# Kernel tuning notes

Measured on AMD Instinct MI355X. Metric: run time of the kernel, lower is better.

The kernel has to match this reference:

```python
import jax, jax.numpy as jnp
import numpy as np

I = 512   # input_size
H = 512   # hidden_size
NH = 2    # num_layers - 1 hidden cells
B = 8
S = 4096

def _unif(k, shape, fan_in):
    bound = 1.0 / np.sqrt(fan_in)
    return jax.random.uniform(k, shape, jnp.float32, -bound, bound)

def setup_inputs() -> dict:
    key = jax.random.key(0)
    ks = jax.random.split(key, 13)
    return {
        "xs": jax.random.normal(ks[0], (B, S, I), jnp.float32),
        # input cell
        "W_xh0": _unif(ks[1], (H, I), I), "b_xh0": _unif(ks[2], (H,), I),
        "W_hh0": _unif(ks[3], (H, H), H), "b_hh0": _unif(ks[4], (H,), H),
        "W_hy0": _unif(ks[5], (H, H), H), "b_hy0": _unif(ks[6], (H,), H),
        # hidden cells, stacked [NH, ...]
        "W_xh_h": _unif(ks[7], (NH, H, H), H), "b_xh_h": _unif(ks[8], (NH, H), H),
        "W_hh_h": _unif(ks[9], (NH, H, H), H), "b_hh_h": _unif(ks[10], (NH, H), H),
        "W_hy_h": _unif(ks[11], (NH, H, H), H), "b_hy_h": _unif(ks[12], (NH, H), H),
    }

def reference(xs, W_xh0, b_xh0, W_hh0, b_hh0, W_hy0, b_hy0,
              W_xh_h, b_xh_h, W_hh_h, b_hh_h, W_hy_h, b_hy_h):
    # NOTE: the original torch forward never passes hs back into the input
    # cell across timesteps (hs is re-zeroed each step), so timesteps are
    # fully independent and we process all (B*S) tokens at once.
    b, s, i = xs.shape
    x = xs.reshape(b * s, i)
    # input cell: hs=0 so W_hh contributes only its bias
    h = jnp.tanh(x @ W_xh0.T + b_xh0 + b_hh0)
    y = h @ W_hy0.T + b_hy0
    # hidden cells (dropout p=0.0 -> identity)
    for li in range(W_xh_h.shape[0]):
        h = jnp.tanh(h @ W_hh_h[li].T + b_hh_h[li] + y @ W_xh_h[li].T + b_xh_h[li])
        y = h @ W_hy_h[li].T + b_hy_h[li]
    outputs = y.reshape(b, s, -1).transpose(1, 0, 2)      # [S, B, H] like torch.stack
    hs_final = h.reshape(b, s, -1)[:, -1, :]              # last timestep, last layer
    return outputs, hs_final
```

## Files before the change

### kernel.cpp

```cpp
#include <hip/hip_runtime.h>
#include <hip/hip_fp16.h>

typedef _Float16 f16;
typedef f16 f16x4 __attribute__((ext_vector_type(4)));
typedef f16 f16x8 __attribute__((ext_vector_type(8)));
typedef float f32x4 __attribute__((ext_vector_type(4)));

#define NTOK 32768
#define KDIM 512
#define SLEN 4096
#define BATCH 8
#define WSZ  262144

#define GLOAD_LDS16(g, l) __builtin_amdgcn_global_load_lds(                 \
    (const __attribute__((address_space(1))) void*)(g),                     \
    (__attribute__((address_space(3))) void*)(l), 16, 0, 0)

__device__ __forceinline__ float fast_tanh(float x) {
    float ax = fabsf(x);
    float t = __expf(-2.0f * ax);
    float r = (1.0f - t) / (1.0f + t);
    return copysignf(r, x);
}

__global__ __launch_bounds__(512, 2)
void chain_kernel(const float* __restrict__ xs,
                  const f16*  __restrict__ Wp,
                  const float* __restrict__ bias,
                  float* __restrict__ out)
{
    __shared__ f16 hbuf[128][512];

    const int tid  = threadIdx.x;
    const int bid  = blockIdx.x;
    const int n0   = bid * 128;
    const int lane = tid & 63;
    const int wave = tid >> 6;
    const int fr   = lane & 15;
    const int q    = lane >> 4;
    const int j0w  = wave * 64;

    {
        const int tk = tid >> 2;
        const int cq = tid & 3;
        const float* __restrict__ src = &xs[(size_t)(n0 + tk) * KDIM];
        #pragma unroll
        for (int kt = 0; kt < 16; ++kt) {
            const int k = kt * 32 + cq * 8;
            const float4 v0 = *(const float4*)&src[k];
            const float4 v1 = *(const float4*)&src[k + 4];
            f16x8 h;
            h[0]=(f16)v0.x; h[1]=(f16)v0.y; h[2]=(f16)v0.z; h[3]=(f16)v0.w;
            h[4]=(f16)v1.x; h[5]=(f16)v1.y; h[6]=(f16)v1.z; h[7]=(f16)v1.w;
            const int c = (k >> 3) ^ (tk & 7);
            *(f16x8*)&hbuf[tk][c << 3] = h;
        }
    }

    f32x4 acc[4][8];

    for (int ph = 0; ph < 3; ++ph) {
        const f16*   __restrict__ wp = Wp + (size_t)ph * WSZ;
        const float* __restrict__ bp = bias + ph * KDIM;
        f32x4 bv[4];
        #pragma unroll
        for (int jt = 0; jt < 4; ++jt)
            bv[jt] = *(const f32x4*)&bp[j0w + jt * 16 + q * 4];
        #pragma unroll
        for (int jt = 0; jt < 4; ++jt)
            #pragma unroll
            for (int mt = 0; mt < 8; ++mt)
                acc[jt][mt] = bv[jt];

        __syncthreads();

        for (int kt = 0; kt < 16; ++kt) {
            f16x8 wf[4], hf[8];
            #pragma unroll
            for (int jt = 0; jt < 4; ++jt)
                wf[jt] = *(const f16x8*)&wp[(size_t)(j0w + jt*16 + fr) * KDIM + kt*32 + q*8];
            #pragma unroll
            for (int mt = 0; mt < 8; ++mt) {
                const int m = mt * 16 + fr;
                const int c = (kt * 4 + q) ^ (m & 7);
                hf[mt] = *(const f16x8*)&hbuf[m][c << 3];
            }
            #pragma unroll
            for (int jt = 0; jt < 4; ++jt)
                #pragma unroll
                for (int mt = 0; mt < 8; ++mt)
                    acc[jt][mt] = __builtin_amdgcn_mfma_f32_16x16x32_f16(
                        wf[jt], hf[mt], acc[jt][mt], 0, 0, 0);
        }

        __syncthreads();

        #pragma unroll
        for (int jt = 0; jt < 4; ++jt) {
            const int j0f  = j0w + jt * 16 + q * 4;
            const int c    = j0f >> 3;
            const int half = j0f & 7;
            #pragma unroll
            for (int mt = 0; mt < 8; ++mt) {
                const int m = mt * 16 + fr;
                f16x4 hv;
                hv[0] = (f16)fast_tanh(acc[jt][mt][0]);
                hv[1] = (f16)fast_tanh(acc[jt][mt][1]);
                hv[2] = (f16)fast_tanh(acc[jt][mt][2]);
                hv[3] = (f16)fast_tanh(acc[jt][mt][3]);
                *(f16x4*)&hbuf[m][((c ^ (m & 7)) << 3) + half] = hv;
            }
        }
    }

    {
        const f16*   __restrict__ wp = Wp + (size_t)3 * WSZ;
        const float* __restrict__ bp = bias + 3 * KDIM;
        f32x4 bv[4];
        #pragma unroll
        for (int jt = 0; jt < 4; ++jt)
            bv[jt] = *(const f32x4*)&bp[j0w + jt * 16 + q * 4];
        #pragma unroll
        for (int jt = 0; jt < 4; ++jt)
            #pragma unroll
            for (int mt = 0; mt < 8; ++mt)
                acc[jt][mt] = bv[jt];

        __syncthreads();

        if ((bid & 31) == 31) {
            const int f = tid;
            const int c = (f >> 3) ^ 7;
            out[(size_t)SLEN * BATCH * KDIM + (size_t)(bid >> 5) * KDIM + f] =
                (float)hbuf[127][(c << 3) + (f & 7)];
        }

        for (int kt = 0; kt < 16; ++kt) {
            f16x8 wf[4], hf[8];
            #pragma unroll
            for (int jt = 0; jt < 4; ++jt)
                wf[jt] = *(const f16x8*)&wp[(size_t)(j0w + jt*16 + fr) * KDIM + kt*32 + q*8];
            #pragma unroll
            for (int mt = 0; mt < 8; ++mt) {
                const int m = mt * 16 + fr;
                const int c = (kt * 4 + q) ^ (m & 7);
                hf[mt] = *(const f16x8*)&hbuf[m][c << 3];
            }
            #pragma unroll
            for (int jt = 0; jt < 4; ++jt)
                #pragma unroll
                for (int mt = 0; mt < 8; ++mt)
                    acc[jt][mt] = __builtin_amdgcn_mfma_f32_16x16x32_f16(
                        wf[jt], hf[mt], acc[jt][mt], 0, 0, 0);
        }

        #pragma unroll
        for (int jt = 0; jt < 4; ++jt) {
            const int j = j0w + jt * 16 + q * 4;
            #pragma unroll
            for (int mt = 0; mt < 8; ++mt) {
                const int n  = n0 + mt * 16 + fr;
                const int s  = n & (SLEN - 1);
                const int bb = n >> 12;
                *(f32x4*)&out[(size_t)(s * BATCH + bb) * KDIM + j] = acc[jt][mt];
            }
        }
    }
}

__global__ __launch_bounds__(256)
void gemm16_fold(const f16* __restrict__ A0, const f16* __restrict__ W0,
                 const float* __restrict__ Cadd0, f16* __restrict__ Cp0)
{
    __shared__ f16 A_s[128][64];
    __shared__ f16 B_s[128][64];

    const int tid  = threadIdx.x;
    const int fold = blockIdx.x >> 4;
    const int bid  = blockIdx.x & 15;
    const size_t off = (size_t)fold * WSZ;
    const f16*   __restrict__ A    = A0 + off;
    const f16*   __restrict__ W    = W0 + off;
    const float* __restrict__ Cadd = Cadd0 + off;
    f16*         __restrict__ Cp   = Cp0 + off;

    const int n0 = (bid >> 2) * 128;
    const int j0 = (bid & 3) * 128;

    const int lane = tid & 63, wave = tid >> 6;
    const int wm = wave >> 1, wn = wave & 1;
    const int fr = lane & 15, q = lane >> 4, sw = fr & 7;
    const int ar8 = lane >> 3;
    const int ach = (lane & 7) ^ ar8;

    f32x4 acc[4][4] = {};

    for (int kt = 0; kt < 8; ++kt) {
        const int k0 = kt * 64;
        #pragma unroll
        for (int p = 0; p < 4; ++p) {
            const int r8 = wave * 32 + p * 8;
            GLOAD_LDS16(&A[(size_t)(n0 + r8 + ar8) * KDIM + k0 + (ach << 3)], &A_s[r8][0]);
            GLOAD_LDS16(&W[(size_t)(j0 + r8 + ar8) * KDIM + k0 + (ach << 3)], &B_s[r8][0]);
        }
        __syncthreads();
        #pragma unroll
        for (int kc = 0; kc < 8; kc += 4) {
            f16x8 a[4], b[4];
            #pragma unroll
            for (int t = 0; t < 4; ++t)
                a[t] = *(const f16x8*)&A_s[wm * 64 + t * 16 + fr][((kc + q) ^ sw) << 3];
            #pragma unroll
            for (int t = 0; t < 4; ++t)
                b[t] = *(const f16x8*)&B_s[wn * 64 + t * 16 + fr][((kc + q) ^ sw) << 3];
            #pragma unroll
            for (int im = 0; im < 4; ++im)
                #pragma unroll
                for (int jn = 0; jn < 4; ++jn)
                    acc[im][jn] = __builtin_amdgcn_mfma_f32_16x16x32_f16(
                        a[im], b[jn], acc[im][jn], 0, 0, 0);
        }
        __syncthreads();
    }

    const int r0 = q * 4, c = fr;
    #pragma unroll
    for (int jn = 0; jn < 4; ++jn) {
        const int j = j0 + wn * 64 + jn * 16 + c;
        #pragma unroll
        for (int im = 0; im < 4; ++im)
            #pragma unroll
            for (int r = 0; r < 4; ++r) {
                const int n = n0 + wm * 64 + im * 16 + r0 + r;
                Cp[(size_t)n * KDIM + j] =
                    (f16)(acc[im][jn][r] + Cadd[(size_t)n * KDIM + j]);
            }
    }
}

__device__ __forceinline__ void cvt2048(const float* __restrict__ src, f16* __restrict__ dst, int t)
{
    const float4 v0 = *(const float4*)&src[(size_t)t * 8];
    const float4 v1 = *(const float4*)&src[(size_t)t * 8 + 4];
    f16x8 h;
    h[0]=(f16)v0.x; h[1]=(f16)v0.y; h[2]=(f16)v0.z; h[3]=(f16)v0.w;
    h[4]=(f16)v1.x; h[5]=(f16)v1.y; h[6]=(f16)v1.z; h[7]=(f16)v1.w;
    *(f16x8*)&dst[(size_t)t * 8] = h;
}

__device__ __forceinline__ void tcvt64(const float* __restrict__ in, f16* __restrict__ out, int b, int tid)
{
    __shared__ float t[64][65];
    const int c0 = (b & 7) * 64, r0 = (b >> 3) * 64;
    const int tr = tid >> 4;
    const int tc = (tid & 15) * 4;
    #pragma unroll
    for (int i = 0; i < 4; ++i) {
        const float4 v = *(const float4*)&in[(size_t)(r0 + tr + 16 * i) * 512 + c0 + tc];
        t[tr + 16 * i][tc + 0] = v.x; t[tr + 16 * i][tc + 1] = v.y;
        t[tr + 16 * i][tc + 2] = v.z; t[tr + 16 * i][tc + 3] = v.w;
    }
    __syncthreads();
    #pragma unroll
    for (int i = 0; i < 4; ++i) {
        const int cl = tr + 16 * i;
        f16x4 h;
        h[0] = (f16)t[tc + 0][cl]; h[1] = (f16)t[tc + 1][cl];
        h[2] = (f16)t[tc + 2][cl]; h[3] = (f16)t[tc + 3][cl];
        *(f16x4*)&out[(size_t)(c0 + cl) * 512 + r0 + tc] = h;
    }
}

__device__ __forceinline__ void bias_matvec(const float* __restrict__ W_xh_h,
                                            const float* __restrict__ b_xh_h,
                                            const float* __restrict__ b_hh_h,
                                            const float* __restrict__ b_hy0,
                                            const float* __restrict__ b_hy_h,
                                            float* __restrict__ bias,
                                            int b, int tid)
{
    const int li   = b >> 3;
    const int lane = tid & 63, wave = tid >> 6;
    const int j0   = (b & 7) * 64 + wave * 16;
    const float* __restrict__ W  = W_xh_h + (size_t)li * WSZ;
    const float* __restrict__ bh = li ? b_hy_h : b_hy0;
    const float4 h0 = *(const float4*)&bh[lane * 8];
    const float4 h1 = *(const float4*)&bh[lane * 8 + 4];
    for (int jj = 0; jj < 16; ++jj) {
        const int j = j0 + jj;
        const float4 w0 = *(const float4*)&W[(size_t)j * 512 + lane * 8];
        const float4 w1 = *(const float4*)&W[(size_t)j * 512 + lane * 8 + 4];
        float s = w0.x*h0.x + w0.y*h0.y + w0.z*h0.z + w0.w*h0.w
                + w1.x*h1.x + w1.y*h1.y + w1.z*h1.z + w1.w*h1.w;
        #pragma unroll
        for (int off = 32; off; off >>= 1) s += __shfl_xor(s, off, 64);
        if (lane == 0)
            bias[(1 + li) * KDIM + j] =
                b_hh_h[li * KDIM + j] + b_xh_h[li * KDIM + j] + s;
    }
}

__global__ __launch_bounds__(256)
void prep_all(const float* __restrict__ W_xh0, const float* __restrict__ W_xh_h,
              const float* __restrict__ W_hy_h, const float* __restrict__ W_hy0,
              const float* __restrict__ b_xh0, const float* __restrict__ b_hh0,
              const float* __restrict__ b_xh_h, const float* __restrict__ b_hh_h,
              const float* __restrict__ b_hy0, const float* __restrict__ b_hy_h,
              f16* __restrict__ Wp, f16* __restrict__ w_xhh, f16* __restrict__ wt,
              float* __restrict__ bias)
{
    const int b = blockIdx.x, tid = threadIdx.x;
    if (b < 128)      cvt2048(W_xh0,            Wp,             b * 256 + tid);
    else if (b < 384) cvt2048(W_xh_h,           w_xhh,          (b - 128) * 256 + tid);
    else if (b < 512) cvt2048(W_hy_h + WSZ,     Wp + 3 * WSZ,   (b - 384) * 256 + tid);
    else if (b < 576) tcvt64(W_hy0,  wt,        b - 512, tid);
    else if (b < 640) tcvt64(W_hy_h, wt + WSZ,  b - 576, tid);
    else if (b < 656) bias_matvec(W_xh_h, b_xh_h, b_hh_h, b_hy0, b_hy_h, bias,
                                  b - 640, tid);
    else {
        const int j = (b - 656) * 256 + tid;
        bias[j] = b_xh0[j] + b_hh0[j];
        bias[3 * KDIM + j] = b_hy_h[KDIM + j];
    }
}

extern "C" void kernel_launch(void* const* d_in, const int* in_sizes, int n_in,
                              void* d_out, int out_size, void* d_ws, size_t ws_size,
                              hipStream_t stream)
{
    (void)in_sizes; (void)n_in; (void)out_size; (void)ws_size;

    const float* xs     = (const float*)d_in[0];
    const float* W_xh0  = (const float*)d_in[1];
    const float* b_xh0  = (const float*)d_in[2];
    const float* b_hh0  = (const float*)d_in[4];
    const float* W_hy0  = (const float*)d_in[5];
    const float* b_hy0  = (const float*)d_in[6];
    const float* W_xh_h = (const float*)d_in[7];
    const float* b_xh_h = (const float*)d_in[8];
    const float* W_hh_h = (const float*)d_in[9];
    const float* b_hh_h = (const float*)d_in[10];
    const float* W_hy_h = (const float*)d_in[11];
    const float* b_hy_h = (const float*)d_in[12];

    f16*   Wp    = (f16*)d_ws;
    f16*   w_xhh = Wp + 4 * WSZ;
    f16*   wt    = w_xhh + 2 * WSZ;
    float* bias  = (float*)(wt + 2 * WSZ);

    dim3 block(256);

    prep_all<<<658, block, 0, stream>>>(W_xh0, W_xh_h, W_hy_h, W_hy0,
                                        b_xh0, b_hh0, b_xh_h, b_hh_h,
                                        b_hy0, b_hy_h, Wp, w_xhh, wt, bias);
    gemm16_fold<<<32, block, 0, stream>>>(w_xhh, wt, W_hh_h, Wp + WSZ);

    chain_kernel<<<256, dim3(512), 0, stream>>>(xs, Wp, bias, (float*)d_out);
}
```

Baseline: 253.8 us.

## Merge prep, weight-fold GEMM and chain into one cooperative kernel

Replaces three separate launches (weight prep/conversion, folded weight GEMM, main chain) with a single cooperative kernel that uses grid-wide syncs between stages. It aims to remove launch gaps and inter-kernel idle time. Prep work is redistributed over 256 blocks of 512 threads, and the fold GEMM is reshaped to 8 waves per block. In exchange it adds two grid barriers, requires all 256 blocks to be co-resident, and leaves most blocks idle during the fold GEMM stage.

```diff
diff --git a/kernel.cpp b/kernel.cpp
--- a/kernel.cpp
+++ b/kernel.cpp
@@ -1,5 +1,8 @@
 #include <hip/hip_runtime.h>
 #include <hip/hip_fp16.h>
+#include <hip/hip_cooperative_groups.h>
+
+namespace cg = cooperative_groups;
 
 typedef _Float16 f16;
 typedef f16 f16x4 __attribute__((ext_vector_type(4)));
@@ -21,221 +24,6 @@
     float t = __expf(-2.0f * ax);
     float r = (1.0f - t) / (1.0f + t);
     return copysignf(r, x);
-}
-
-__global__ __launch_bounds__(512, 2)
-void chain_kernel(const float* __restrict__ xs,
-                  const f16*  __restrict__ Wp,
-                  const float* __restrict__ bias,
-                  float* __restrict__ out)
-{
-    __shared__ f16 hbuf[128][512];
-
-    const int tid  = threadIdx.x;
-    const int bid  = blockIdx.x;
-    const int n0   = bid * 128;
-    const int lane = tid & 63;
-    const int wave = tid >> 6;
-    const int fr   = lane & 15;
-    const int q    = lane >> 4;
-    const int j0w  = wave * 64;
-
-    {
-        const int tk = tid >> 2;
-        const int cq = tid & 3;
-        const float* __restrict__ src = &xs[(size_t)(n0 + tk) * KDIM];
-        #pragma unroll
-        for (int kt = 0; kt < 16; ++kt) {
-            const int k = kt * 32 + cq * 8;
-            const float4 v0 = *(const float4*)&src[k];
-            const float4 v1 = *(const float4*)&src[k + 4];
-            f16x8 h;
-            h[0]=(f16)v0.x; h[1]=(f16)v0.y; h[2]=(f16)v0.z; h[3]=(f16)v0.w;
-            h[4]=(f16)v1.x; h[5]=(f16)v1.y; h[6]=(f16)v1.z; h[7]=(f16)v1.w;
-            const int c = (k >> 3) ^ (tk & 7);
-            *(f16x8*)&hbuf[tk][c << 3] = h;
-        }
-    }
-
-    f32x4 acc[4][8];
-
-    for (int ph = 0; ph < 3; ++ph) {
-        const f16*   __restrict__ wp = Wp + (size_t)ph * WSZ;
-        const float* __restrict__ bp = bias + ph * KDIM;
-        f32x4 bv[4];
-        #pragma unroll
-        for (int jt = 0; jt < 4; ++jt)
-            bv[jt] = *(const f32x4*)&bp[j0w + jt * 16 + q * 4];
-        #pragma unroll
-        for (int jt = 0; jt < 4; ++jt)
-            #pragma unroll
-            for (int mt = 0; mt < 8; ++mt)
-                acc[jt][mt] = bv[jt];
-
-        __syncthreads();
-
-        for (int kt = 0; kt < 16; ++kt) {
-            f16x8 wf[4], hf[8];
-            #pragma unroll
-            for (int jt = 0; jt < 4; ++jt)
-                wf[jt] = *(const f16x8*)&wp[(size_t)(j0w + jt*16 + fr) * KDIM + kt*32 + q*8];
-            #pragma unroll
-            for (int mt = 0; mt < 8; ++mt) {
-                const int m = mt * 16 + fr;
-                const int c = (kt * 4 + q) ^ (m & 7);
-                hf[mt] = *(const f16x8*)&hbuf[m][c << 3];
-            }
-            #pragma unroll
-            for (int jt = 0; jt < 4; ++jt)
-                #pragma unroll
-                for (int mt = 0; mt < 8; ++mt)
-                    acc[jt][mt] = __builtin_amdgcn_mfma_f32_16x16x32_f16(
-                        wf[jt], hf[mt], acc[jt][mt], 0, 0, 0);
-        }
-
-        __syncthreads();
-
-        #pragma unroll
-        for (int jt = 0; jt < 4; ++jt) {
-            const int j0f  = j0w + jt * 16 + q * 4;
-            const int c    = j0f >> 3;
-            const int half = j0f & 7;
-            #pragma unroll
-            for (int mt = 0; mt < 8; ++mt) {
-                const int m = mt * 16 + fr;
-                f16x4 hv;
-                hv[0] = (f16)fast_tanh(acc[jt][mt][0]);
-                hv[1] = (f16)fast_tanh(acc[jt][mt][1]);
-                hv[2] = (f16)fast_tanh(acc[jt][mt][2]);
-                hv[3] = (f16)fast_tanh(acc[jt][mt][3]);
-                *(f16x4*)&hbuf[m][((c ^ (m & 7)) << 3) + half] = hv;
-            }
-        }
-    }
-
-    {
-        const f16*   __restrict__ wp = Wp + (size_t)3 * WSZ;
-        const float* __restrict__ bp = bias + 3 * KDIM;
-        f32x4 bv[4];
-        #pragma unroll
-        for (int jt = 0; jt < 4; ++jt)
-            bv[jt] = *(const f32x4*)&bp[j0w + jt * 16 + q * 4];
-        #pragma unroll
-        for (int jt = 0; jt < 4; ++jt)
-            #pragma unroll
-            for (int mt = 0; mt < 8; ++mt)
-                acc[jt][mt] = bv[jt];
-
-        __syncthreads();
-
-        if ((bid & 31) == 31) {
-            const int f = tid;
-            const int c = (f >> 3) ^ 7;
-            out[(size_t)SLEN * BATCH * KDIM + (size_t)(bid >> 5) * KDIM + f] =
-                (float)hbuf[127][(c << 3) + (f & 7)];
-        }
-
-        for (int kt = 0; kt < 16; ++kt) {
-            f16x8 wf[4], hf[8];
-            #pragma unroll
-            for (int jt = 0; jt < 4; ++jt)
-                wf[jt] = *(const f16x8*)&wp[(size_t)(j0w + jt*16 + fr) * KDIM + kt*32 + q*8];
-            #pragma unroll
-            for (int mt = 0; mt < 8; ++mt) {
-                const int m = mt * 16 + fr;
-                const int c = (kt * 4 + q) ^ (m & 7);
-                hf[mt] = *(const f16x8*)&hbuf[m][c << 3];
-            }
-            #pragma unroll
-            for (int jt = 0; jt < 4; ++jt)
-                #pragma unroll
-                for (int mt = 0; mt < 8; ++mt)
-                    acc[jt][mt] = __builtin_amdgcn_mfma_f32_16x16x32_f16(
-                        wf[jt], hf[mt], acc[jt][mt], 0, 0, 0);
-        }
-
-        #pragma unroll
-        for (int jt = 0; jt < 4; ++jt) {
-            const int j = j0w + jt * 16 + q * 4;
-            #pragma unroll
-            for (int mt = 0; mt < 8; ++mt) {
-                const int n  = n0 + mt * 16 + fr;
-                const int s  = n & (SLEN - 1);
-                const int bb = n >> 12;
-                *(f32x4*)&out[(size_t)(s * BATCH + bb) * KDIM + j] = acc[jt][mt];
-            }
-        }
-    }
-}
-
-__global__ __launch_bounds__(256)
-void gemm16_fold(const f16* __restrict__ A0, const f16* __restrict__ W0,
-                 const float* __restrict__ Cadd0, f16* __restrict__ Cp0)
-{
-    __shared__ f16 A_s[128][64];
-    __shared__ f16 B_s[128][64];
-
-    const int tid  = threadIdx.x;
-    const int fold = blockIdx.x >> 4;
-    const int bid  = blockIdx.x & 15;
-    const size_t off = (size_t)fold * WSZ;
-    const f16*   __restrict__ A    = A0 + off;
-    const f16*   __restrict__ W    = W0 + off;
-    const float* __restrict__ Cadd = Cadd0 + off;
-    f16*         __restrict__ Cp   = Cp0 + off;
-
-    const int n0 = (bid >> 2) * 128;
-    const int j0 = (bid & 3) * 128;
-
-    const int lane = tid & 63, wave = tid >> 6;
-    const int wm = wave >> 1, wn = wave & 1;
-    const int fr = lane & 15, q = lane >> 4, sw = fr & 7;
-    const int ar8 = lane >> 3;
-    const int ach = (lane & 7) ^ ar8;
-
-    f32x4 acc[4][4] = {};
-
-    for (int kt = 0; kt < 8; ++kt) {
-        const int k0 = kt * 64;
-        #pragma unroll
-        for (int p = 0; p < 4; ++p) {
-            const int r8 = wave * 32 + p * 8;
-            GLOAD_LDS16(&A[(size_t)(n0 + r8 + ar8) * KDIM + k0 + (ach << 3)], &A_s[r8][0]);
-            GLOAD_LDS16(&W[(size_t)(j0 + r8 + ar8) * KDIM + k0 + (ach << 3)], &B_s[r8][0]);
-        }
-        __syncthreads();
-        #pragma unroll
-        for (int kc = 0; kc < 8; kc += 4) {
-            f16x8 a[4], b[4];
-            #pragma unroll
-            for (int t = 0; t < 4; ++t)
-                a[t] = *(const f16x8*)&A_s[wm * 64 + t * 16 + fr][((kc + q) ^ sw) << 3];
-            #pragma unroll
-            for (int t = 0; t < 4; ++t)
-                b[t] = *(const f16x8*)&B_s[wn * 64 + t * 16 + fr][((kc + q) ^ sw) << 3];
-            #pragma unroll
-            for (int im = 0; im < 4; ++im)
-                #pragma unroll
-                for (int jn = 0; jn < 4; ++jn)
-                    acc[im][jn] = __builtin_amdgcn_mfma_f32_16x16x32_f16(
-                        a[im], b[jn], acc[im][jn], 0, 0, 0);
-        }
-        __syncthreads();
-    }
-
-    const int r0 = q * 4, c = fr;
-    #pragma unroll
-    for (int jn = 0; jn < 4; ++jn) {
-        const int j = j0 + wn * 64 + jn * 16 + c;
-        #pragma unroll
-        for (int im = 0; im < 4; ++im)
-            #pragma unroll
-            for (int r = 0; r < 4; ++r) {
-                const int n = n0 + wm * 64 + im * 16 + r0 + r;
-                Cp[(size_t)n * KDIM + j] =
-                    (f16)(acc[im][jn][r] + Cadd[(size_t)n * KDIM + j]);
-            }
-    }
 }
 
 __device__ __forceinline__ void cvt2048(const float* __restrict__ src, f16* __restrict__ dst, int t)
@@ -248,22 +36,23 @@
     *(f16x8*)&dst[(size_t)t * 8] = h;
 }
 
-__device__ __forceinline__ void tcvt64(const float* __restrict__ in, f16* __restrict__ out, int b, int tid)
+__device__ __forceinline__ void tcvt64_512(const float* __restrict__ in, f16* __restrict__ out,
+                                           int tile, int tid, float (*t)[65])
 {
-    __shared__ float t[64][65];
-    const int c0 = (b & 7) * 64, r0 = (b >> 3) * 64;
+    const int c0 = (tile & 7) * 64, r0 = (tile >> 3) * 64;
     const int tr = tid >> 4;
     const int tc = (tid & 15) * 4;
     #pragma unroll
-    for (int i = 0; i < 4; ++i) {
-        const float4 v = *(const float4*)&in[(size_t)(r0 + tr + 16 * i) * 512 + c0 + tc];
-        t[tr + 16 * i][tc + 0] = v.x; t[tr + 16 * i][tc + 1] = v.y;
-        t[tr + 16 * i][tc + 2] = v.z; t[tr + 16 * i][tc + 3] = v.w;
+    for (int i = 0; i < 2; ++i) {
+        const int row = tr + 32 * i;
+        const float4 v = *(const float4*)&in[(size_t)(r0 + row) * 512 + c0 + tc];
+        t[row][tc + 0] = v.x; t[row][tc + 1] = v.y;
+        t[row][tc + 2] = v.z; t[row][tc + 3] = v.w;
     }
     __syncthreads();
     #pragma unroll
-    for (int i = 0; i < 4; ++i) {
-        const int cl = tr + 16 * i;
+    for (int i = 0; i < 2; ++i) {
+        const int cl = tr + 32 * i;
         f16x4 h;
         h[0] = (f16)t[tc + 0][cl]; h[1] = (f16)t[tc + 1][cl];
         h[2] = (f16)t[tc + 2][cl]; h[3] = (f16)t[tc + 3][cl];
@@ -271,56 +60,265 @@
     }
 }
 
-__device__ __forceinline__ void bias_matvec(const float* __restrict__ W_xh_h,
-                                            const float* __restrict__ b_xh_h,
-                                            const float* __restrict__ b_hh_h,
-                                            const float* __restrict__ b_hy0,
-                                            const float* __restrict__ b_hy_h,
-                                            float* __restrict__ bias,
-                                            int b, int tid)
+__global__ __launch_bounds__(512, 2)
+void mega_kernel(const float* __restrict__ xs,
+                 const float* __restrict__ W_xh0, const float* __restrict__ b_xh0,
+                 const float* __restrict__ b_hh0, const float* __restrict__ W_hy0,
+                 const float* __restrict__ b_hy0, const float* __restrict__ W_xh_h,
+                 const float* __restrict__ b_xh_h, const float* __restrict__ W_hh_h,
+                 const float* __restrict__ b_hh_h, const float* __restrict__ W_hy_h,
+                 const float* __restrict__ b_hy_h,
+                 float* __restrict__ out,
+                 f16* __restrict__ Wp, f16* __restrict__ w_xhh,
+                 f16* __restrict__ wt, float* __restrict__ bias)
 {
-    const int li   = b >> 3;
-    const int lane = tid & 63, wave = tid >> 6;
-    const int j0   = (b & 7) * 64 + wave * 16;
-    const float* __restrict__ W  = W_xh_h + (size_t)li * WSZ;
-    const float* __restrict__ bh = li ? b_hy_h : b_hy0;
-    const float4 h0 = *(const float4*)&bh[lane * 8];
-    const float4 h1 = *(const float4*)&bh[lane * 8 + 4];
-    for (int jj = 0; jj < 16; ++jj) {
-        const int j = j0 + jj;
-        const float4 w0 = *(const float4*)&W[(size_t)j * 512 + lane * 8];
-        const float4 w1 = *(const float4*)&W[(size_t)j * 512 + lane * 8 + 4];
-        float s = w0.x*h0.x + w0.y*h0.y + w0.z*h0.z + w0.w*h0.w
-                + w1.x*h1.x + w1.y*h1.y + w1.z*h1.z + w1.w*h1.w;
+    __shared__ __align__(16) char smem[131072];
+
+    const int tid  = threadIdx.x;
+    const int bid  = blockIdx.x;
+    const int lane = tid & 63;
+    const int wave = tid >> 6;
+
+    {
+        const int t = bid * 512 + tid;
+        if (t < 32768)       cvt2048(W_xh0,        Wp,           t);
+        else if (t < 98304)  cvt2048(W_xh_h,       w_xhh,        t - 32768);
+        else                 cvt2048(W_hy_h + WSZ, Wp + 3 * WSZ, t - 98304);
+
+        if (bid < 128) {
+            float (*ttr)[65] = (float(*)[65])smem;
+            if (bid < 64) tcvt64_512(W_hy0,  wt,       bid,      tid, ttr);
+            else          tcvt64_512(W_hy_h, wt + WSZ, bid - 64, tid, ttr);
+        } else if (bid < 192) {
+            const int gw = (bid - 128) * 8 + wave;
+            const int jg = gw * 2;
+            const int li = jg >> 9;
+            const int jb = jg & 511;
+            const float* __restrict__ W  = W_xh_h + (size_t)li * WSZ;
+            const float* __restrict__ bh = li ? b_hy_h : b_hy0;
+            const float4 h0 = *(const float4*)&bh[lane * 8];
+            const float4 h1 = *(const float4*)&bh[lane * 8 + 4];
+            #pragma unroll
+            for (int u = 0; u < 2; ++u) {
+                const int j = jb + u;
+                const float4 w0 = *(const float4*)&W[(size_t)j * 512 + lane * 8];
+                const float4 w1 = *(const float4*)&W[(size_t)j * 512 + lane * 8 + 4];
+                float s = w0.x*h0.x + w0.y*h0.y + w0.z*h0.z + w0.w*h0.w
+                        + w1.x*h1.x + w1.y*h1.y + w1.z*h1.z + w1.w*h1.w;
+                #pragma unroll
+                for (int off = 32; off; off >>= 1) s += __shfl_xor(s, off, 64);
+                if (lane == 0)
+                    bias[(1 + li) * KDIM + j] =
+                        b_hh_h[li * KDIM + j] + b_xh_h[li * KDIM + j] + s;
+            }
+        } else if (bid == 192) {
+            bias[tid] = b_xh0[tid] + b_hh0[tid];
+            bias[3 * KDIM + tid] = b_hy_h[KDIM + tid];
+        }
+    }
+
+    cg::this_grid().sync();
+
+    if (bid < 32) {
+        f16 (*A_s)[64] = (f16(*)[64])smem;
+        f16 (*B_s)[64] = (f16(*)[64])(smem + 16384);
+
+        const int fold = bid >> 4;
+        const int fb   = bid & 15;
+        const size_t off = (size_t)fold * WSZ;
+        const f16*   __restrict__ A    = w_xhh + off;
+        const f16*   __restrict__ W    = wt + off;
+        const float* __restrict__ Cadd = W_hh_h + off;
+        f16*         __restrict__ Cp   = Wp + WSZ + off;
+
+        const int n0 = (fb >> 2) * 128;
+        const int j0 = (fb & 3) * 128;
+        const int wm = wave >> 2, wn = wave & 3;
+        const int fr = lane & 15, q = lane >> 4, sw = fr & 7;
+        const int ar8 = lane >> 3;
+        const int ach = (lane & 7) ^ ar8;
+
+        f32x4 acc[4][2] = {};
+
+        for (int kt = 0; kt < 8; ++kt) {
+            const int k0 = kt * 64;
+            #pragma unroll
+            for (int p = 0; p < 2; ++p) {
+                const int r8 = wave * 16 + p * 8;
+                GLOAD_LDS16(&A[(size_t)(n0 + r8 + ar8) * KDIM + k0 + (ach << 3)], &A_s[r8][0]);
+                GLOAD_LDS16(&W[(size_t)(j0 + r8 + ar8) * KDIM + k0 + (ach << 3)], &B_s[r8][0]);
+            }
+            __syncthreads();
+            #pragma unroll
+            for (int kc = 0; kc < 8; kc += 4) {
+                f16x8 a[4], b[2];
+                #pragma unroll
+                for (int t = 0; t < 4; ++t)
+                    a[t] = *(const f16x8*)&A_s[wm * 64 + t * 16 + fr][((kc + q) ^ sw) << 3];
+                #pragma unroll
+                for (int t = 0; t < 2; ++t)
+                    b[t] = *(const f16x8*)&B_s[wn * 32 + t * 16 + fr][((kc + q) ^ sw) << 3];
+                #pragma unroll
+                for (int im = 0; im < 4; ++im)
+                    #pragma unroll
+                    for (int jn = 0; jn < 2; ++jn)
+                        acc[im][jn] = __builtin_amdgcn_mfma_f32_16x16x32_f16(
+                            a[im], b[jn], acc[im][jn], 0, 0, 0);
+            }
+            __syncthreads();
+        }
+
+        const int r0 = q * 4;
         #pragma unroll
-        for (int off = 32; off; off >>= 1) s += __shfl_xor(s, off, 64);
-        if (lane == 0)
-            bias[(1 + li) * KDIM + j] =
-                b_hh_h[li * KDIM + j] + b_xh_h[li * KDIM + j] + s;
-    }
-}
-
-__global__ __launch_bounds__(256)
-void prep_all(const float* __restrict__ W_xh0, const float* __restrict__ W_xh_h,
-              const float* __restrict__ W_hy_h, const float* __restrict__ W_hy0,
-              const float* __restrict__ b_xh0, const float* __restrict__ b_hh0,
-              const float* __restrict__ b_xh_h, const float* __restrict__ b_hh_h,
-              const float* __restrict__ b_hy0, const float* __restrict__ b_hy_h,
-              f16* __restrict__ Wp, f16* __restrict__ w_xhh, f16* __restrict__ wt,
-              float* __restrict__ bias)
-{
-    const int b = blockIdx.x, tid = threadIdx.x;
-    if (b < 128)      cvt2048(W_xh0,            Wp,             b * 256 + tid);
-    else if (b < 384) cvt2048(W_xh_h,           w_xhh,          (b - 128) * 256 + tid);
-    else if (b < 512) cvt2048(W_hy_h + WSZ,     Wp + 3 * WSZ,   (b - 384) * 256 + tid);
-    else if (b < 576) tcvt64(W_hy0,  wt,        b - 512, tid);
-    else if (b < 640) tcvt64(W_hy_h, wt + WSZ,  b - 576, tid);
-    else if (b < 656) bias_matvec(W_xh_h, b_xh_h, b_hh_h, b_hy0, b_hy_h, bias,
-                                  b - 640, tid);
-    else {
-        const int j = (b - 656) * 256 + tid;
-        bias[j] = b_xh0[j] + b_hh0[j];
-        bias[3 * KDIM + j] = b_hy_h[KDIM + j];
+        for (int jn = 0; jn < 2; ++jn) {
+            const int j = j0 + wn * 32 + jn * 16 + fr;
+            #pragma unroll
+            for (int im = 0; im < 4; ++im)
+                #pragma unroll
+                for (int r = 0; r < 4; ++r) {
+                    const int n = n0 + wm * 64 + im * 16 + r0 + r;
+                    Cp[(size_t)n * KDIM + j] =
+                        (f16)(acc[im][jn][r] + Cadd[(size_t)n * KDIM + j]);
+                }
+        }
+    }
+
+    cg::this_grid().sync();
+
+    {
+        f16 (*hbuf)[512] = (f16(*)[512])smem;
+
+        const int n0  = bid * 128;
+        const int fr  = lane & 15;
+        const int q   = lane >> 4;
+        const int j0w = wave * 64;
+
+        {
+            const int tk = tid >> 2;
+            const int cq = tid & 3;
+            const float* __restrict__ src = &xs[(size_t)(n0 + tk) * KDIM];
+            #pragma unroll
+            for (int kt = 0; kt < 16; ++kt) {
+                const int k = kt * 32 + cq * 8;
+                const float4 v0 = *(const float4*)&src[k];
+                const float4 v1 = *(const float4*)&src[k + 4];
+                f16x8 h;
+                h[0]=(f16)v0.x; h[1]=(f16)v0.y; h[2]=(f16)v0.z; h[3]=(f16)v0.w;
+                h[4]=(f16)v1.x; h[5]=(f16)v1.y; h[6]=(f16)v1.z; h[7]=(f16)v1.w;
+                const int c = (k >> 3) ^ (tk & 7);
+                *(f16x8*)&hbuf[tk][c << 3] = h;
+            }
+        }
+
+        f32x4 acc[4][8];
+
+        for (int ph = 0; ph < 3; ++ph) {
+            const f16*   __restrict__ wp = Wp + (size_t)ph * WSZ;
+            const float* __restrict__ bp = bias + ph * KDIM;
+            f32x4 bv[4];
+            #pragma unroll
+            for (int jt = 0; jt < 4; ++jt)
+                bv[jt] = *(const f32x4*)&bp[j0w + jt * 16 + q * 4];
+            #pragma unroll
+            for (int jt = 0; jt < 4; ++jt)
+                #pragma unroll
+                for (int mt = 0; mt < 8; ++mt)
+                    acc[jt][mt] = bv[jt];
+
+            __syncthreads();
+
+            for (int kt = 0; kt < 16; ++kt) {
+                f16x8 wf[4], hf[8];
+                #pragma unroll
+                for (int jt = 0; jt < 4; ++jt)
+                    wf[jt] = *(const f16x8*)&wp[(size_t)(j0w + jt*16 + fr) * KDIM + kt*32 + q*8];
+                #pragma unroll
+                for (int mt = 0; mt < 8; ++mt) {
+                    const int m = mt * 16 + fr;
+                    const int c = (kt * 4 + q) ^ (m & 7);
+                    hf[mt] = *(const f16x8*)&hbuf[m][c << 3];
+                }
+                #pragma unroll
+                for (int jt = 0; jt < 4; ++jt)
+                    #pragma unroll
+                    for (int mt = 0; mt < 8; ++mt)
+                        acc[jt][mt] = __builtin_amdgcn_mfma_f32_16x16x32_f16(
+                            wf[jt], hf[mt], acc[jt][mt], 0, 0, 0);
+            }
+
+            __syncthreads();
+
+            #pragma unroll
+            for (int jt = 0; jt < 4; ++jt) {
+                const int j0f  = j0w + jt * 16 + q * 4;
+                const int c    = j0f >> 3;
+                const int half = j0f & 7;
+                #pragma unroll
+                for (int mt = 0; mt < 8; ++mt) {
+                    const int m = mt * 16 + fr;
+                    f16x4 hv;
+                    hv[0] = (f16)fast_tanh(acc[jt][mt][0]);
+                    hv[1] = (f16)fast_tanh(acc[jt][mt][1]);
+                    hv[2] = (f16)fast_tanh(acc[jt][mt][2]);
+                    hv[3] = (f16)fast_tanh(acc[jt][mt][3]);
+                    *(f16x4*)&hbuf[m][((c ^ (m & 7)) << 3) + half] = hv;
+                }
+            }
+        }
+
+        {
+            const f16*   __restrict__ wp = Wp + (size_t)3 * WSZ;
+            const float* __restrict__ bp = bias + 3 * KDIM;
+            f32x4 bv[4];
+            #pragma unroll
+            for (int jt = 0; jt < 4; ++jt)
+                bv[jt] = *(const f32x4*)&bp[j0w + jt * 16 + q * 4];
+            #pragma unroll
+            for (int jt = 0; jt < 4; ++jt)
+                #pragma unroll
+                for (int mt = 0; mt < 8; ++mt)
+                    acc[jt][mt] = bv[jt];
+
+            __syncthreads();
+
+            if ((bid & 31) == 31) {
+                const int f = tid;
+                const int c = (f >> 3) ^ 7;
+                out[(size_t)SLEN * BATCH * KDIM + (size_t)(bid >> 5) * KDIM + f] =
+                    (float)hbuf[127][(c << 3) + (f & 7)];
+            }
+
+            for (int kt = 0; kt < 16; ++kt) {
+                f16x8 wf[4], hf[8];
+                #pragma unroll
+                for (int jt = 0; jt < 4; ++jt)
+                    wf[jt] = *(const f16x8*)&wp[(size_t)(j0w + jt*16 + fr) * KDIM + kt*32 + q*8];
+                #pragma unroll
+                for (int mt = 0; mt < 8; ++mt) {
+                    const int m = mt * 16 + fr;
+                    const int c = (kt * 4 + q) ^ (m & 7);
+                    hf[mt] = *(const f16x8*)&hbuf[m][c << 3];
+                }
+                #pragma unroll
+                for (int jt = 0; jt < 4; ++jt)
+                    #pragma unroll
+                    for (int mt = 0; mt < 8; ++mt)
+                        acc[jt][mt] = __builtin_amdgcn_mfma_f32_16x16x32_f16(
+                            wf[jt], hf[mt], acc[jt][mt], 0, 0, 0);
+            }
+
+            #pragma unroll
+            for (int jt = 0; jt < 4; ++jt) {
+                const int j = j0w + jt * 16 + q * 4;
+                #pragma unroll
+                for (int mt = 0; mt < 8; ++mt) {
+                    const int n  = n0 + mt * 16 + fr;
+                    const int s  = n & (SLEN - 1);
+                    const int bb = n >> 12;
+                    *(f32x4*)&out[(size_t)(s * BATCH + bb) * KDIM + j] = acc[jt][mt];
+                }
+            }
+        }
     }
 }
 
@@ -342,18 +340,18 @@
     const float* b_hh_h = (const float*)d_in[10];
     const float* W_hy_h = (const float*)d_in[11];
     const float* b_hy_h = (const float*)d_in[12];
+    float*       outp   = (float*)d_out;
 
     f16*   Wp    = (f16*)d_ws;
     f16*   w_xhh = Wp + 4 * WSZ;
     f16*   wt    = w_xhh + 2 * WSZ;
     float* bias  = (float*)(wt + 2 * WSZ);
 
-    dim3 block(256);
-
-    prep_all<<<658, block, 0, stream>>>(W_xh0, W_xh_h, W_hy_h, W_hy0,
-                                        b_xh0, b_hh0, b_xh_h, b_hh_h,
-                                        b_hy0, b_hy_h, Wp, w_xhh, wt, bias);
-    gemm16_fold<<<32, block, 0, stream>>>(w_xhh, wt, W_hh_h, Wp + WSZ);
-
-    chain_kernel<<<256, dim3(512), 0, stream>>>(xs, Wp, bias, (float*)d_out);
-}
+    void* args[] = { (void*)&xs, (void*)&W_xh0, (void*)&b_xh0, (void*)&b_hh0,
+                     (void*)&W_hy0, (void*)&b_hy0, (void*)&W_xh_h, (void*)&b_xh_h,
+                     (void*)&W_hh_h, (void*)&b_hh_h, (void*)&W_hy_h, (void*)&b_hy_h,
+                     (void*)&outp, (void*)&Wp, (void*)&w_xhh, (void*)&wt, (void*)&bias };
+
+    hipLaunchCooperativeKernel((const void*)mega_kernel, dim3(256), dim3(512),
+                               args, 0, stream);
+}
```

Result: slower. 329.0 us (+29.6%).
